# Optimization experiments

Hardware: AMD Instinct MI355X
Metric: run time of the kernel (lower is better)

## Reference

```python
import jax, jax.numpy as jnp
import numpy as np

B, S, H, D = 8, 1024, 16, 64
W = H * D  # hidden width = 1024


def setup_inputs() -> dict:
    key = jax.random.key(0)
    ks = jax.random.split(key, 5)
    std = 0.02
    return {
        "from_tensor": jax.random.normal(ks[0], (B, S, W), dtype=jnp.float32),
        "to_tensor": jax.random.normal(ks[1], (B, S, W), dtype=jnp.float32),
        "Wq": jax.random.normal(ks[2], (W, W), dtype=jnp.float32) * std,
        "bq": jnp.zeros((W,), dtype=jnp.float32),
        "Wk": jax.random.normal(ks[3], (W, W), dtype=jnp.float32) * std,
        "bk": jnp.zeros((W,), dtype=jnp.float32),
        "Wv": jax.random.normal(ks[4], (W, W), dtype=jnp.float32) * std,
        "bv": jnp.zeros((W,), dtype=jnp.float32),
    }


def reference(from_tensor, to_tensor, Wq, bq, Wk, bk, Wv, bv):
    # Q/K/V projections (no activations: query_act=key_act=value_act=None)
    q = from_tensor @ Wq + bq  # [B, S, W]
    k = to_tensor @ Wk + bk
    v = to_tensor @ Wv + bv
    # split heads -> [B, H, S, D]
    q = q.reshape(B, S, H, D).transpose(0, 2, 1, 3)
    k = k.reshape(B, S, H, D).transpose(0, 2, 1, 3)
    v = v.reshape(B, S, H, D).transpose(0, 2, 1, 3)
    scale = 1.0 / np.sqrt(float(D))
    scores = jnp.einsum("bhqd,bhkd->bhqk", q, k) * scale  # [B, H, S, S]
    # attention_mask=None, dropout_prob=0.0 -> no mask, no dropout
    probs = jax.nn.softmax(scores, axis=-1)
    ctx = jnp.einsum("bhqk,bhkd->bhqd", probs, v)  # [B, H, S, D]
    # merge heads -> [B, S, H*D] (do_return_2d_tensor=False)
    return ctx.transpose(0, 2, 1, 3).reshape(B, S, H * D)
```

## Files before the change

### kernel.cpp

```cpp
#include <hip/hip_runtime.h>
#include <hip/hip_bf16.h>
#include <math.h>


#define B_ 8
#define S_ 1024
#define H_ 16
#define D_ 64
#define W_ 1024

typedef __bf16 bf16x8 __attribute__((ext_vector_type(8)));
typedef float f32x4 __attribute__((ext_vector_type(4)));
typedef unsigned short ushort_t;

#define MFMA16(a, b, c) __builtin_amdgcn_mfma_f32_16x16x32_bf16((a), (b), (c), 0, 0, 0)

__device__ inline ushort_t f2bf(float f) {
    unsigned int u = __float_as_uint(f);
    u += 0x7fff + ((u >> 16) & 1);
    return (ushort_t)(u >> 16);
}

__device__ inline ushort_t f2bf_rhu(float f) {
    return (ushort_t)((__float_as_uint(f) + 0x8000u) >> 16);
}

__device__ inline void async16(const void* g, void* l) {
    __builtin_amdgcn_global_load_lds((const __attribute__((address_space(1))) void*)g,
                                     (__attribute__((address_space(3))) void*)l, 16, 0, 0);
}

__global__ __launch_bounds__(256) void cast_bf16_kernel(const float* __restrict__ src,
                                                        ushort_t* __restrict__ dst, int n4) {
    int i = blockIdx.x * 256 + threadIdx.x;
    if (i >= n4) return;
    float4 v = ((const float4*)src)[i];
    ushort4 o;
    o.x = f2bf(v.x); o.y = f2bf(v.y); o.z = f2bf(v.z); o.w = f2bf(v.w);
    ((ushort4*)dst)[i] = o;
}

__global__ __launch_bounds__(256) void transpose_cast(const float* __restrict__ Wq,
                                                      const float* __restrict__ Wk,
                                                      const float* __restrict__ Wv,
                                                      ushort_t* __restrict__ Wt) {
    __shared__ float tile[32][33];
    int z = blockIdx.z;
    const float* src = (z == 0) ? Wq : (z == 1 ? Wk : Wv);
    ushort_t* dst = Wt + (size_t)z * W_ * W_;
    int tx = threadIdx.x, ty = threadIdx.y;
    int x = blockIdx.x * 32 + tx;
#pragma unroll
    for (int jj = 0; jj < 4; jj++) {
        int y = blockIdx.y * 32 + ty + jj * 8;
        tile[ty + jj * 8][tx] = src[(size_t)y * W_ + x];
    }
    __syncthreads();
    int x2 = blockIdx.y * 32 + tx;
#pragma unroll
    for (int jj = 0; jj < 4; jj++) {
        int y2 = blockIdx.x * 32 + ty + jj * 8;
        dst[(size_t)y2 * W_ + x2] = f2bf(tile[tx][ty + jj * 8]);
    }
}

__global__ __launch_bounds__(256) void qkv_gemm(const ushort_t* __restrict__ fromB,
                                                const ushort_t* __restrict__ toB,
                                                const ushort_t* __restrict__ Wt,
                                                const float* __restrict__ bq,
                                                const float* __restrict__ bk,
                                                const float* __restrict__ bv,
                                                ushort_t* __restrict__ Qd,
                                                ushort_t* __restrict__ Kd,
                                                ushort_t* __restrict__ Vt) {
    __shared__ __attribute__((aligned(16))) ushort_t As[128 * 32];
    __shared__ __attribute__((aligned(16))) ushort_t Bs[128 * 32];
    int z = blockIdx.z;
    const ushort_t* A = (z == 0) ? fromB : toB;
    const ushort_t* Bt = Wt + (size_t)z * (W_ * W_);
    const float* bias = (z == 0) ? bq : (z == 1 ? bk : bv);
    ushort_t* dst = (z == 0) ? Qd : (z == 1 ? Kd : Vt);

    int t = threadIdx.x;
    int lane = t & 63, w = t >> 6;
    int wm = w >> 1, wn = w & 1;
    int ln = lane & 15, qd = lane >> 4;
    int mBase = blockIdx.y * 128, nBase = blockIdx.x * 128;
    int wb = t & ~63;

    f32x4 zero = {0.f, 0.f, 0.f, 0.f};
    f32x4 acc[4][4];
#pragma unroll
    for (int i = 0; i < 4; i++)
#pragma unroll
        for (int j = 0; j < 4; j++) acc[i][j] = zero;

    for (int kt = 0; kt < 32; ++kt) {
        int k0 = kt * 32;
#pragma unroll
        for (int c = 0; c < 2; ++c) {
            int idx16 = c * 256 + t;
            int row = idx16 >> 2, seg = idx16 & 3;
            async16(A + (size_t)(mBase + row) * W_ + k0 + seg * 8, As + (size_t)(c * 256 + wb) * 8);
            async16(Bt + (size_t)(nBase + row) * W_ + k0 + seg * 8, Bs + (size_t)(c * 256 + wb) * 8);
        }
        __syncthreads();
        bf16x8 af[4], bfr[4];
#pragma unroll
        for (int i = 0; i < 4; i++) af[i] = *(const bf16x8*)(As + (wm * 64 + i * 16 + ln) * 32 + qd * 8);
#pragma unroll
        for (int j = 0; j < 4; j++) bfr[j] = *(const bf16x8*)(Bs + (wn * 64 + j * 16 + ln) * 32 + qd * 8);
#pragma unroll
        for (int i = 0; i < 4; i++)
#pragma unroll
            for (int j = 0; j < 4; j++) acc[i][j] = MFMA16(af[i], bfr[j], acc[i][j]);
        __syncthreads();
    }

#pragma unroll
    for (int j = 0; j < 4; j++) {
        int n = nBase + wn * 64 + j * 16 + ln;
        float bb = bias[n];
        int h = n >> 6, d = n & 63;
#pragma unroll
        for (int i = 0; i < 4; i++) {
            int mrow = mBase + wm * 64 + i * 16 + qd * 4;
#pragma unroll
            for (int r = 0; r < 4; r++) {
                int m = mrow + r;
                int b = m >> 10, s = m & 1023;
                float v = acc[i][j][r] + bb;
                if (z == 0) v *= 0.18033688011111773f;
                size_t idx;
                if (z < 2) idx = ((size_t)(b * H_ + h) * S_ + s) * D_ + d;
                else       idx = ((size_t)(b * H_ + h) * D_ + d) * S_ + s;
                dst[idx] = f2bf(v);
            }
        }
    }
}

__global__ __launch_bounds__(256, 3) void attn(const ushort_t* __restrict__ Qd,
                                               const ushort_t* __restrict__ Kd,
                                               const ushort_t* __restrict__ Vt,
                                               float* __restrict__ out) {
    __shared__ __attribute__((aligned(16))) ushort_t Ks[2][4096];
    __shared__ __attribute__((aligned(16))) ushort_t Vs[2][4096];
    __shared__ __attribute__((aligned(16))) ushort_t Plds[4][32][72];

    int bh = blockIdx.y;
    int t = threadIdx.x, w = t >> 6, lane = t & 63;
    int ln = lane & 15, qd = lane >> 4;
    int qbase = blockIdx.x * 128 + w * 32;
    const ushort_t* Qb = Qd + (size_t)bh * S_ * D_;
    const ushort_t* Kb = Kd + (size_t)bh * S_ * D_;
    const ushort_t* Vb = Vt + (size_t)bh * D_ * S_;

    bf16x8 qf[2][2];
#pragma unroll
    for (int i = 0; i < 2; i++) {
        const ushort_t* qp = Qb + (size_t)(qbase + i * 16 + ln) * D_ + qd * 8;
        qf[i][0] = *(const bf16x8*)qp;
        qf[i][1] = *(const bf16x8*)(qp + 32);
    }

    int l8 = lane >> 3, s8 = lane & 7;
    int stgOff = (s8 ^ l8) << 3;
    const ushort_t* kg = Kb + (size_t)(w * 16 + l8) * D_ + stgOff;
    const ushort_t* vg = Vb + (size_t)(w * 16 + l8) * S_ + stgOff;
    int kOff = ln * 64 + ((qd ^ (ln & 7)) << 3);

    float rs[2][4];
    f32x4 zero = {0.f, 0.f, 0.f, 0.f};
    f32x4 accO[2][4];
#pragma unroll
    for (int i = 0; i < 2; i++) {
        rs[i][0] = rs[i][1] = rs[i][2] = rs[i][3] = 0.f;
#pragma unroll
        for (int jd = 0; jd < 4; jd++) accO[i][jd] = zero;
    }

    async16(kg, &Ks[0][w * 1024]);
    async16(kg + 8 * D_, &Ks[0][w * 1024 + 512]);
    async16(vg, &Vs[0][w * 1024]);
    async16(vg + 8 * S_, &Vs[0][w * 1024 + 512]);

    for (int c = 0; c < 16; ++c) {
        int buf = c & 1;
        __builtin_amdgcn_s_waitcnt(0x0F70);
        __syncthreads();
        if (c + 1 < 16) {
            int kc = (c + 1) * 64;
            async16(kg + (size_t)kc * D_, &Ks[buf ^ 1][w * 1024]);
            async16(kg + (size_t)kc * D_ + 8 * D_, &Ks[buf ^ 1][w * 1024 + 512]);
            async16(vg + kc, &Vs[buf ^ 1][w * 1024]);
            async16(vg + kc + 8 * S_, &Vs[buf ^ 1][w * 1024 + 512]);
        }

        f32x4 sc[2][4];
#pragma unroll
        for (int i = 0; i < 2; i++)
#pragma unroll
            for (int j = 0; j < 4; j++) sc[i][j] = zero;
#pragma unroll
        for (int j = 0; j < 4; j++) {
            bf16x8 k0 = *(const bf16x8*)&Ks[buf][j * 1024 + kOff];
            bf16x8 k1 = *(const bf16x8*)&Ks[buf][(j * 1024 + kOff) ^ 32];
#pragma unroll
            for (int i = 0; i < 2; i++) {
                sc[i][j] = MFMA16(qf[i][0], k0, sc[i][j]);
                sc[i][j] = MFMA16(qf[i][1], k1, sc[i][j]);
            }
        }
#pragma unroll
        for (int i = 0; i < 2; i++)
#pragma unroll
            for (int j = 0; j < 4; j++)
#pragma unroll
                for (int r = 0; r < 4; r++) {
                    float p = exp2f(sc[i][j][r]);
                    rs[i][r] += p;
                    Plds[w][i * 16 + qd * 4 + r][j * 16 + ln] = f2bf_rhu(p);
                }
        bf16x8 pf[2][2];
#pragma unroll
        for (int i = 0; i < 2; i++) {
            pf[i][0] = *(const bf16x8*)&Plds[w][i * 16 + ln][qd * 8];
            pf[i][1] = *(const bf16x8*)&Plds[w][i * 16 + ln][32 + qd * 8];
        }
#pragma unroll
        for (int jd = 0; jd < 4; jd++) {
            bf16x8 v0 = *(const bf16x8*)&Vs[buf][jd * 1024 + kOff];
            bf16x8 v1 = *(const bf16x8*)&Vs[buf][(jd * 1024 + kOff) ^ 32];
#pragma unroll
            for (int i = 0; i < 2; i++) {
                accO[i][jd] = MFMA16(pf[i][0], v0, accO[i][jd]);
                accO[i][jd] = MFMA16(pf[i][1], v1, accO[i][jd]);
            }
        }
    }

    int b = bh >> 4, h = bh & 15;
#pragma unroll
    for (int i = 0; i < 2; i++)
#pragma unroll
        for (int r = 0; r < 4; r++) {
            float s = rs[i][r];
            s += __shfl_xor(s, 1);
            s += __shfl_xor(s, 2);
            s += __shfl_xor(s, 4);
            s += __shfl_xor(s, 8);
            float inv = 1.f / s;
            int q = qbase + i * 16 + qd * 4 + r;
            float* op = out + ((size_t)(b * S_ + q) * H_ + h) * D_;
#pragma unroll
            for (int jd = 0; jd < 4; jd++) op[jd * 16 + ln] = accO[i][jd][r] * inv;
        }
}

extern "C" void kernel_launch(void* const* d_in, const int* in_sizes, int n_in,
                              void* d_out, int out_size, void* d_ws, size_t ws_size,
                              hipStream_t stream) {
    const float* from = (const float*)d_in[0];
    const float* to_  = (const float*)d_in[1];
    const float* Wq = (const float*)d_in[2];
    const float* bq = (const float*)d_in[3];
    const float* Wk = (const float*)d_in[4];
    const float* bk = (const float*)d_in[5];
    const float* Wv = (const float*)d_in[6];
    const float* bv = (const float*)d_in[7];
    float* out = (float*)d_out;

    const size_t NTOK = (size_t)B_ * S_ * W_;
    ushort_t* ws = (ushort_t*)d_ws;
    ushort_t* fromB = ws;
    ushort_t* toB = fromB + NTOK;
    ushort_t* Wt = toB + NTOK;
    ushort_t* Qd = Wt + (size_t)3 * W_ * W_;
    ushort_t* Kd = Qd + NTOK;
    ushort_t* Vt = Kd + NTOK;

    int n4 = (int)(NTOK / 4);
    cast_bf16_kernel<<<dim3(n4 / 256), dim3(256), 0, stream>>>(from, fromB, n4);
    cast_bf16_kernel<<<dim3(n4 / 256), dim3(256), 0, stream>>>(to_, toB, n4);
    transpose_cast<<<dim3(32, 32, 3), dim3(32, 8), 0, stream>>>(Wq, Wk, Wv, Wt);
    qkv_gemm<<<dim3(8, 64, 3), dim3(256), 0, stream>>>(fromB, toB, Wt, bq, bk, bv, Qd, Kd, Vt);
    attn<<<dim3(8, 128), dim3(256), 0, stream>>>(Qd, Kd, Vt, out);
}
```

Before: 283.1 us.

## Double-buffer QKV GEMM with swizzled LDS, remap tiles, fuse casts, add setprio

The QKV GEMM now double-buffers its A/B LDS tiles and prefetches the next k-slice while computing the current one, which removes one barrier per iteration. LDS reads use an XOR swizzle to reduce bank conflicts, and the block index is remapped to a different M/N tile order for cache locality. The two input casts are merged into one launch, and s_setprio raises wave priority around the MFMA sections in both the GEMM and attention kernels. Double buffering doubles LDS use in the GEMM, which could lower occupancy.

```diff
diff --git a/kernel.cpp b/kernel.cpp
--- a/kernel.cpp
+++ b/kernel.cpp
@@ -30,10 +30,14 @@
                                      (__attribute__((address_space(3))) void*)l, 16, 0, 0);
 }
 
-__global__ __launch_bounds__(256) void cast_bf16_kernel(const float* __restrict__ src,
-                                                        ushort_t* __restrict__ dst, int n4) {
+__global__ __launch_bounds__(256) void cast2_bf16(const float* __restrict__ a,
+                                                  const float* __restrict__ b,
+                                                  ushort_t* __restrict__ da,
+                                                  ushort_t* __restrict__ db, int n4) {
     int i = blockIdx.x * 256 + threadIdx.x;
     if (i >= n4) return;
+    const float* src = blockIdx.y ? b : a;
+    ushort_t* dst = blockIdx.y ? db : da;
     float4 v = ((const float4*)src)[i];
     ushort4 o;
     o.x = f2bf(v.x); o.y = f2bf(v.y); o.z = f2bf(v.z); o.w = f2bf(v.w);
@@ -73,20 +77,37 @@
                                                 ushort_t* __restrict__ Qd,
                                                 ushort_t* __restrict__ Kd,
                                                 ushort_t* __restrict__ Vt) {
-    __shared__ __attribute__((aligned(16))) ushort_t As[128 * 32];
-    __shared__ __attribute__((aligned(16))) ushort_t Bs[128 * 32];
-    int z = blockIdx.z;
+    __shared__ __attribute__((aligned(16))) ushort_t As[2][128 * 32];
+    __shared__ __attribute__((aligned(16))) ushort_t Bs[2][128 * 32];
+    int z = blockIdx.y;
     const ushort_t* A = (z == 0) ? fromB : toB;
     const ushort_t* Bt = Wt + (size_t)z * (W_ * W_);
     const float* bias = (z == 0) ? bq : (z == 1 ? bk : bv);
     ushort_t* dst = (z == 0) ? Qd : (z == 1 ? Kd : Vt);
 
+    int bx = blockIdx.x;
+    int j64 = bx >> 3;
+    int mTile = ((bx & 7) << 3) | (j64 >> 3);
+    int nTile = j64 & 7;
+    int mBase = mTile * 128, nBase = nTile * 128;
+
     int t = threadIdx.x;
     int lane = t & 63, w = t >> 6;
     int wm = w >> 1, wn = w & 1;
     int ln = lane & 15, qd = lane >> 4;
-    int mBase = blockIdx.y * 128, nBase = blockIdx.x * 128;
     int wb = t & ~63;
+    int swz = (qd ^ (ln & 3)) << 3;
+
+    int row0 = t >> 2;
+    int segG0 = ((t & 3) ^ (row0 & 3)) << 3;
+    int row1 = (256 + t) >> 2;
+    int segG1 = ((t & 3) ^ (row1 & 3)) << 3;
+    const ushort_t* ga0 = A + (size_t)(mBase + row0) * W_ + segG0;
+    const ushort_t* ga1 = A + (size_t)(mBase + row1) * W_ + segG1;
+    const ushort_t* gb0 = Bt + (size_t)(nBase + row0) * W_ + segG0;
+    const ushort_t* gb1 = Bt + (size_t)(nBase + row1) * W_ + segG1;
+    int ldst0 = wb * 8;
+    int ldst1 = (256 + wb) * 8;
 
     f32x4 zero = {0.f, 0.f, 0.f, 0.f};
     f32x4 acc[4][4];
@@ -95,26 +116,33 @@
 #pragma unroll
         for (int j = 0; j < 4; j++) acc[i][j] = zero;
 
+    async16(ga0, &As[0][ldst0]);
+    async16(gb0, &Bs[0][ldst0]);
+    async16(ga1, &As[0][ldst1]);
+    async16(gb1, &Bs[0][ldst1]);
+
     for (int kt = 0; kt < 32; ++kt) {
-        int k0 = kt * 32;
-#pragma unroll
-        for (int c = 0; c < 2; ++c) {
-            int idx16 = c * 256 + t;
-            int row = idx16 >> 2, seg = idx16 & 3;
-            async16(A + (size_t)(mBase + row) * W_ + k0 + seg * 8, As + (size_t)(c * 256 + wb) * 8);
-            async16(Bt + (size_t)(nBase + row) * W_ + k0 + seg * 8, Bs + (size_t)(c * 256 + wb) * 8);
-        }
+        int buf = kt & 1;
+        __builtin_amdgcn_s_waitcnt(0x0F70);
         __syncthreads();
+        if (kt + 1 < 32) {
+            int k0 = (kt + 1) * 32;
+            async16(ga0 + k0, &As[buf ^ 1][ldst0]);
+            async16(gb0 + k0, &Bs[buf ^ 1][ldst0]);
+            async16(ga1 + k0, &As[buf ^ 1][ldst1]);
+            async16(gb1 + k0, &Bs[buf ^ 1][ldst1]);
+        }
         bf16x8 af[4], bfr[4];
 #pragma unroll
-        for (int i = 0; i < 4; i++) af[i] = *(const bf16x8*)(As + (wm * 64 + i * 16 + ln) * 32 + qd * 8);
-#pragma unroll
-        for (int j = 0; j < 4; j++) bfr[j] = *(const bf16x8*)(Bs + (wn * 64 + j * 16 + ln) * 32 + qd * 8);
+        for (int i = 0; i < 4; i++) af[i] = *(const bf16x8*)(&As[buf][(wm * 64 + i * 16 + ln) * 32 + swz]);
+#pragma unroll
+        for (int j = 0; j < 4; j++) bfr[j] = *(const bf16x8*)(&Bs[buf][(wn * 64 + j * 16 + ln) * 32 + swz]);
+        __builtin_amdgcn_s_setprio(1);
 #pragma unroll
         for (int i = 0; i < 4; i++)
 #pragma unroll
             for (int j = 0; j < 4; j++) acc[i][j] = MFMA16(af[i], bfr[j], acc[i][j]);
-        __syncthreads();
+        __builtin_amdgcn_s_setprio(0);
     }
 
 #pragma unroll
@@ -202,6 +230,7 @@
         for (int i = 0; i < 2; i++)
 #pragma unroll
             for (int j = 0; j < 4; j++) sc[i][j] = zero;
+        __builtin_amdgcn_s_setprio(1);
 #pragma unroll
         for (int j = 0; j < 4; j++) {
             bf16x8 k0 = *(const bf16x8*)&Ks[buf][j * 1024 + kOff];
@@ -212,6 +241,7 @@
                 sc[i][j] = MFMA16(qf[i][1], k1, sc[i][j]);
             }
         }
+        __builtin_amdgcn_s_setprio(0);
 #pragma unroll
         for (int i = 0; i < 2; i++)
 #pragma unroll
@@ -228,6 +258,7 @@
             pf[i][0] = *(const bf16x8*)&Plds[w][i * 16 + ln][qd * 8];
             pf[i][1] = *(const bf16x8*)&Plds[w][i * 16 + ln][32 + qd * 8];
         }
+        __builtin_amdgcn_s_setprio(1);
 #pragma unroll
         for (int jd = 0; jd < 4; jd++) {
             bf16x8 v0 = *(const bf16x8*)&Vs[buf][jd * 1024 + kOff];
@@ -238,6 +269,7 @@
                 accO[i][jd] = MFMA16(pf[i][1], v1, accO[i][jd]);
             }
         }
+        __builtin_amdgcn_s_setprio(0);
     }
 
     int b = bh >> 4, h = bh & 15;
@@ -281,9 +313,8 @@
     ushort_t* Vt = Kd + NTOK;
 
     int n4 = (int)(NTOK / 4);
-    cast_bf16_kernel<<<dim3(n4 / 256), dim3(256), 0, stream>>>(from, fromB, n4);
-    cast_bf16_kernel<<<dim3(n4 / 256), dim3(256), 0, stream>>>(to_, toB, n4);
+    cast2_bf16<<<dim3(n4 / 256, 2), dim3(256), 0, stream>>>(from, to_, fromB, toB, n4);
     transpose_cast<<<dim3(32, 32, 3), dim3(32, 8), 0, stream>>>(Wq, Wk, Wv, Wt);
-    qkv_gemm<<<dim3(8, 64, 3), dim3(256), 0, stream>>>(fromB, toB, Wt, bq, bk, bv, Qd, Kd, Vt);
+    qkv_gemm<<<dim3(512, 3), dim3(256), 0, stream>>>(fromB, toB, Wt, bq, bk, bv, Qd, Kd, Vt);
     attn<<<dim3(8, 128), dim3(256), 0, stream>>>(Qd, Kd, Vt, out);
 }
```

After: 274.8 us. -2.9%, faster.
